# Optimization experiments

Measured on AMD Instinct MI355X. Metric: run time of the kernel, lower is better.

The kernel has to match this reference:

```python
import jax, jax.numpy as jnp
import numpy as np

BLOCK_SIZE = 128  # init_kwargs block_size


def setup_inputs() -> dict:
    key = jax.random.key(0)
    kq, kk, kv = jax.random.split(key, 3)
    shape = (8, 16, 4096, 128)  # [B, H, L, D]
    q = jax.random.normal(kq, shape, dtype=jnp.float32)
    k = jax.random.normal(kk, shape, dtype=jnp.float32)
    v = jax.random.normal(kv, shape, dtype=jnp.float32)
    return {"q": q, "k": k, "v": v}


def reference(q, k, v):
    # Block-diagonal local attention. The torch code builds a dense [L,L]
    # score matrix filled with -10000 off the block diagonal; exp(-10000)
    # underflows to exactly 0 in fp32 after max-subtraction, so the dense
    # softmax is mathematically identical to per-block softmax. We honor
    # the block sparsity and never materialize the L x L matrix.
    w = BLOCK_SIZE
    B, H, L, D = q.shape
    nb = L // w
    qb = q.reshape(B, H, nb, w, D)
    kb = k.reshape(B, H, nb, w, D)
    vb = v.reshape(B, H, nb, w, D)
    # NOTE: original applies NO 1/sqrt(D) scaling.
    score = jnp.einsum('bhnwd,bhnud->bhnwu', qb, kb)   # [B,H,nb,w,w]
    probs = jax.nn.softmax(score, axis=-1)
    out = jnp.einsum('bhnwu,bhnud->bhnwd', probs, vb)
    return out.reshape(B, H, L, D)
```

## Files before the change

kernel.cpp:

```cpp
#include <hip/hip_runtime.h>

typedef _Float16 half8  __attribute__((ext_vector_type(8)));
typedef _Float16 half4v __attribute__((ext_vector_type(4)));
typedef float    f32x4  __attribute__((ext_vector_type(4)));

__device__ __forceinline__ int swz(int row) {
    return ((row ^ (row >> 3)) & 15) << 4;
}

__global__ __launch_bounds__(512, 4) void battn_kernel(
    const float* __restrict__ Q, const float* __restrict__ K,
    const float* __restrict__ V, float* __restrict__ O)
{
    extern __shared__ __align__(16) char smem[];
    const int tid  = threadIdx.x;
    const int lane = tid & 63;
    const int w    = tid >> 6;
    const int la   = lane & 15;
    const int u    = lane >> 4;
    const size_t base = (size_t)blockIdx.x * (128 * 128);

    const float* Qb = Q + base;
    const float* Kb = K + base;
    const float* Vb = V + base;
    float*       Ob = O + base;

    float4 kreg[8];
#pragma unroll
    for (int it = 0; it < 8; ++it)
        kreg[it] = *(const float4*)(Kb + it * 2048 + tid * 4);

    half8 qfrag[4];
    {
        const float* qrow = Qb + (w * 16 + la) * 128;
#pragma unroll
        for (int kk = 0; kk < 4; ++kk) {
            const float4 a = *(const float4*)(qrow + kk * 32 + u * 8);
            const float4 b = *(const float4*)(qrow + kk * 32 + u * 8 + 4);
            qfrag[kk][0] = (_Float16)a.x; qfrag[kk][1] = (_Float16)a.y;
            qfrag[kk][2] = (_Float16)a.z; qfrag[kk][3] = (_Float16)a.w;
            qfrag[kk][4] = (_Float16)b.x; qfrag[kk][5] = (_Float16)b.y;
            qfrag[kk][6] = (_Float16)b.z; qfrag[kk][7] = (_Float16)b.w;
        }
    }
#pragma unroll
    for (int it = 0; it < 8; ++it) {
        const int idx = it * 2048 + tid * 4;
        const int row = idx >> 7;
        const int col = idx & 127;
        half4v h;
        h[0] = (_Float16)kreg[it].x; h[1] = (_Float16)kreg[it].y;
        h[2] = (_Float16)kreg[it].z; h[3] = (_Float16)kreg[it].w;
        int byte = row * 256 + col * 2;
        byte ^= swz(row);
        *(half4v*)(smem + byte) = h;
    }
    __syncthreads();

    float vld[32];
#pragma unroll
    for (int kk = 0; kk < 4; ++kk)
#pragma unroll
        for (int i = 0; i < 8; ++i)
            vld[kk * 8 + i] = Vb[(kk * 32 + u * 8 + i) * 128 + w * 16 + la];
    __builtin_amdgcn_sched_barrier(0);

    f32x4 acc[8];
#pragma unroll
    for (int t = 0; t < 8; ++t) acc[t] = (f32x4){0.f, 0.f, 0.f, 0.f};
#pragma unroll
    for (int t = 0; t < 8; ++t) {
#pragma unroll
        for (int kk = 0; kk < 4; ++kk) {
            const int row = t * 16 + la;
            int byte = row * 256 + kk * 64 + u * 16;
            byte ^= swz(row);
            const half8 kf = *(const half8*)(smem + byte);
            acc[t] = __builtin_amdgcn_mfma_f32_16x16x32_f16(qfrag[kk], kf, acc[t], 0, 0, 0);
        }
    }

    float inv[4];
#pragma unroll
    for (int r = 0; r < 4; ++r) {
        float m = acc[0][r];
#pragma unroll
        for (int t = 1; t < 8; ++t) m = fmaxf(m, acc[t][r]);
        m = fmaxf(m, __shfl_xor(m, 1));
        m = fmaxf(m, __shfl_xor(m, 2));
        m = fmaxf(m, __shfl_xor(m, 4));
        m = fmaxf(m, __shfl_xor(m, 8));
        float s = 0.f;
#pragma unroll
        for (int t = 0; t < 8; ++t) {
            const float e = __expf(acc[t][r] - m);
            acc[t][r] = e;
            s += e;
        }
        s += __shfl_xor(s, 1);
        s += __shfl_xor(s, 2);
        s += __shfl_xor(s, 4);
        s += __shfl_xor(s, 8);
        inv[r] = 1.0f / s;
    }

    half8 vfrag[4];
#pragma unroll
    for (int kk = 0; kk < 4; ++kk)
#pragma unroll
        for (int i = 0; i < 8; ++i)
            vfrag[kk][i] = (_Float16)vld[kk * 8 + i];

#pragma unroll
    for (int t = 0; t < 8; ++t) {
#pragma unroll
        for (int r = 0; r < 4; ++r) {
            const int q   = w * 16 + u * 4 + r;
            const int col = t * 16 + la;
            int byte = 32768 + q * 256 + col * 2;
            byte ^= swz(q & 15);
            *(_Float16*)(smem + byte) = (_Float16)(acc[t][r] * inv[r]);
        }
    }
    __syncthreads();

#pragma unroll
    for (int qt = 0; qt < 8; ++qt) {
        half8 pb[4];
#pragma unroll
        for (int kk = 0; kk < 4; ++kk) {
            int byte = 32768 + (qt * 16 + la) * 256 + kk * 64 + u * 16;
            byte ^= swz(la);
            pb[kk] = *(const half8*)(smem + byte);
        }
        f32x4 oa = (f32x4){0.f, 0.f, 0.f, 0.f};
#pragma unroll
        for (int kk = 0; kk < 4; ++kk)
            oa = __builtin_amdgcn_mfma_f32_16x16x32_f16(vfrag[kk], pb[kk], oa, 0, 0, 0);
        *(float4*)(Ob + (qt * 16 + la) * 128 + w * 16 + u * 4) =
            make_float4(oa[0], oa[1], oa[2], oa[3]);
    }
}

extern "C" void kernel_launch(void* const* d_in, const int* in_sizes, int n_in,
                              void* d_out, int out_size, void* d_ws, size_t ws_size,
                              hipStream_t stream) {
    const float* q = (const float*)d_in[0];
    const float* k = (const float*)d_in[1];
    const float* v = (const float*)d_in[2];
    float* o = (float*)d_out;
    const int nblocks = in_sizes[0] / (128 * 128);
    battn_kernel<<<dim3(nblocks), dim3(512), 65536, stream>>>(q, k, v, o);
}
```

Measured before the change: 214.7 us.

## Make workgroups loop over 16 blocks with register prefetch of next Q/K

Each workgroup now processes 16 consecutive 128x128 attention blocks in a loop instead of one. While the current block is computed, the next block's Q and K are loaded into registers with inline-asm global loads, gated by hand-placed s_waitcnt vmcnt counts. The goal is to hide global-load latency and amortize launch and setup cost. In exchange the grid shrinks to about one workgroup per CU, launch bounds drop to 2 blocks per CU, and shared memory becomes static. That leaves less wave-level parallelism to cover memory latency, and correctness depends on the manual vmcnt bookkeeping.

```diff
diff --git a/kernel.cpp b/kernel.cpp
--- a/kernel.cpp
+++ b/kernel.cpp
@@ -4,141 +4,192 @@
 typedef _Float16 half4v __attribute__((ext_vector_type(4)));
 typedef float    f32x4  __attribute__((ext_vector_type(4)));
 
+#define ITER 16
+
 __device__ __forceinline__ int swz(int row) {
     return ((row ^ (row >> 3)) & 15) << 4;
 }
 
-__global__ __launch_bounds__(512, 4) void battn_kernel(
+__device__ __forceinline__ half8 cvt_pair(f32x4 a, f32x4 b) {
+    half8 h;
+    h[0] = (_Float16)a[0]; h[1] = (_Float16)a[1]; h[2] = (_Float16)a[2]; h[3] = (_Float16)a[3];
+    h[4] = (_Float16)b[0]; h[5] = (_Float16)b[1]; h[6] = (_Float16)b[2]; h[7] = (_Float16)b[3];
+    return h;
+}
+
+__global__ __launch_bounds__(512, 2) void battn_kernel(
     const float* __restrict__ Q, const float* __restrict__ K,
     const float* __restrict__ V, float* __restrict__ O)
 {
-    extern __shared__ __align__(16) char smem[];
+    __shared__ __align__(16) char smem[65536];
     const int tid  = threadIdx.x;
     const int lane = tid & 63;
     const int w    = tid >> 6;
     const int la   = lane & 15;
     const int u    = lane >> 4;
-    const size_t base = (size_t)blockIdx.x * (128 * 128);
-
-    const float* Qb = Q + base;
-    const float* Kb = K + base;
-    const float* Vb = V + base;
-    float*       Ob = O + base;
-
-    float4 kreg[8];
-#pragma unroll
-    for (int it = 0; it < 8; ++it)
-        kreg[it] = *(const float4*)(Kb + it * 2048 + tid * 4);
-
+
+    const size_t base0 = (size_t)blockIdx.x * ITER * (128 * 128);
+
+    f32x4 kreg[8];
+    f32x4 qld[8];
+    float vld[32];
     half8 qfrag[4];
+
     {
-        const float* qrow = Qb + (w * 16 + la) * 128;
+        const float* qrow = Q + base0 + (w * 16 + la) * 128;
 #pragma unroll
         for (int kk = 0; kk < 4; ++kk) {
-            const float4 a = *(const float4*)(qrow + kk * 32 + u * 8);
-            const float4 b = *(const float4*)(qrow + kk * 32 + u * 8 + 4);
-            qfrag[kk][0] = (_Float16)a.x; qfrag[kk][1] = (_Float16)a.y;
-            qfrag[kk][2] = (_Float16)a.z; qfrag[kk][3] = (_Float16)a.w;
-            qfrag[kk][4] = (_Float16)b.x; qfrag[kk][5] = (_Float16)b.y;
-            qfrag[kk][6] = (_Float16)b.z; qfrag[kk][7] = (_Float16)b.w;
+            const float* p0 = qrow + kk * 32 + u * 8;
+            asm volatile("global_load_dwordx4 %0, %1, off" : "=v"(qld[2 * kk])     : "v"(p0));
+            asm volatile("global_load_dwordx4 %0, %1, off" : "=v"(qld[2 * kk + 1]) : "v"(p0 + 4));
+        }
+        const float* kptr = K + base0 + tid * 4;
+#pragma unroll
+        for (int it = 0; it < 8; ++it) {
+            const float* p = kptr + it * 2048;
+            asm volatile("global_load_dwordx4 %0, %1, off" : "=v"(kreg[it]) : "v"(p));
         }
     }
-#pragma unroll
-    for (int it = 0; it < 8; ++it) {
-        const int idx = it * 2048 + tid * 4;
-        const int row = idx >> 7;
-        const int col = idx & 127;
-        half4v h;
-        h[0] = (_Float16)kreg[it].x; h[1] = (_Float16)kreg[it].y;
-        h[2] = (_Float16)kreg[it].z; h[3] = (_Float16)kreg[it].w;
-        int byte = row * 256 + col * 2;
-        byte ^= swz(row);
-        *(half4v*)(smem + byte) = h;
-    }
-    __syncthreads();
-
-    float vld[32];
-#pragma unroll
-    for (int kk = 0; kk < 4; ++kk)
-#pragma unroll
-        for (int i = 0; i < 8; ++i)
-            vld[kk * 8 + i] = Vb[(kk * 32 + u * 8 + i) * 128 + w * 16 + la];
+    asm volatile("s_waitcnt vmcnt(8)" ::: "memory");
     __builtin_amdgcn_sched_barrier(0);
-
-    f32x4 acc[8];
-#pragma unroll
-    for (int t = 0; t < 8; ++t) acc[t] = (f32x4){0.f, 0.f, 0.f, 0.f};
-#pragma unroll
-    for (int t = 0; t < 8; ++t) {
-#pragma unroll
-        for (int kk = 0; kk < 4; ++kk) {
+#pragma unroll
+    for (int kk = 0; kk < 4; ++kk) qfrag[kk] = cvt_pair(qld[2 * kk], qld[2 * kk + 1]);
+    asm volatile("s_waitcnt vmcnt(0)" ::: "memory");
+    __builtin_amdgcn_sched_barrier(0);
+
+    for (int i = 0; i < ITER; ++i) {
+        const size_t base  = base0 + (size_t)i * (128 * 128);
+        const size_t nbase = base0 + (size_t)(i + 1 < ITER ? i + 1 : i) * (128 * 128);
+        float* Ob = O + base;
+
+#pragma unroll
+        for (int it = 0; it < 8; ++it) {
+            const int idx = it * 2048 + tid * 4;
+            const int row = idx >> 7;
+            const int col = idx & 127;
+            half4v h;
+            h[0] = (_Float16)kreg[it][0]; h[1] = (_Float16)kreg[it][1];
+            h[2] = (_Float16)kreg[it][2]; h[3] = (_Float16)kreg[it][3];
+            int byte = row * 256 + col * 2;
+            byte ^= swz(row);
+            *(half4v*)(smem + byte) = h;
+        }
+
+        {
+            const float* vbase = V + base + w * 16 + la;
+#pragma unroll
+            for (int kk = 0; kk < 4; ++kk)
+#pragma unroll
+                for (int t2 = 0; t2 < 8; ++t2) {
+                    const float* p = vbase + (kk * 32 + u * 8 + t2) * 128;
+                    asm volatile("global_load_dword %0, %1, off"
+                                 : "=v"(vld[kk * 8 + t2]) : "v"(p));
+                }
+        }
+        {
+            const float* qrow = Q + nbase + (w * 16 + la) * 128;
+#pragma unroll
+            for (int kk = 0; kk < 4; ++kk) {
+                const float* p0 = qrow + kk * 32 + u * 8;
+                asm volatile("global_load_dwordx4 %0, %1, off" : "=v"(qld[2 * kk])     : "v"(p0));
+                asm volatile("global_load_dwordx4 %0, %1, off" : "=v"(qld[2 * kk + 1]) : "v"(p0 + 4));
+            }
+            const float* kptr = K + nbase + tid * 4;
+#pragma unroll
+            for (int it = 0; it < 8; ++it) {
+                const float* p = kptr + it * 2048;
+                asm volatile("global_load_dwordx4 %0, %1, off" : "=v"(kreg[it]) : "v"(p));
+            }
+        }
+        __builtin_amdgcn_sched_barrier(0);
+
+        __syncthreads();
+
+        f32x4 acc[8];
+#pragma unroll
+        for (int t = 0; t < 8; ++t) acc[t] = (f32x4){0.f, 0.f, 0.f, 0.f};
+#pragma unroll
+        for (int t = 0; t < 8; ++t) {
             const int row = t * 16 + la;
-            int byte = row * 256 + kk * 64 + u * 16;
-            byte ^= swz(row);
-            const half8 kf = *(const half8*)(smem + byte);
-            acc[t] = __builtin_amdgcn_mfma_f32_16x16x32_f16(qfrag[kk], kf, acc[t], 0, 0, 0);
-        }
-    }
-
-    float inv[4];
-#pragma unroll
-    for (int r = 0; r < 4; ++r) {
-        float m = acc[0][r];
-#pragma unroll
-        for (int t = 1; t < 8; ++t) m = fmaxf(m, acc[t][r]);
-        m = fmaxf(m, __shfl_xor(m, 1));
-        m = fmaxf(m, __shfl_xor(m, 2));
-        m = fmaxf(m, __shfl_xor(m, 4));
-        m = fmaxf(m, __shfl_xor(m, 8));
-        float s = 0.f;
+#pragma unroll
+            for (int kk = 0; kk < 4; ++kk) {
+                int byte = row * 256 + kk * 64 + u * 16;
+                byte ^= swz(row);
+                const half8 kf = *(const half8*)(smem + byte);
+                acc[t] = __builtin_amdgcn_mfma_f32_16x16x32_f16(qfrag[kk], kf, acc[t], 0, 0, 0);
+            }
+        }
+
+        float inv[4];
+#pragma unroll
+        for (int r = 0; r < 4; ++r) {
+            float m = acc[0][r];
+#pragma unroll
+            for (int t = 1; t < 8; ++t) m = fmaxf(m, acc[t][r]);
+            m = fmaxf(m, __shfl_xor(m, 1));
+            m = fmaxf(m, __shfl_xor(m, 2));
+            m = fmaxf(m, __shfl_xor(m, 4));
+            m = fmaxf(m, __shfl_xor(m, 8));
+            float s = 0.f;
+#pragma unroll
+            for (int t = 0; t < 8; ++t) {
+                const float e = __expf(acc[t][r] - m);
+                acc[t][r] = e;
+                s += e;
+            }
+            s += __shfl_xor(s, 1);
+            s += __shfl_xor(s, 2);
+            s += __shfl_xor(s, 4);
+            s += __shfl_xor(s, 8);
+            inv[r] = 1.0f / s;
+        }
+
 #pragma unroll
         for (int t = 0; t < 8; ++t) {
-            const float e = __expf(acc[t][r] - m);
-            acc[t][r] = e;
-            s += e;
-        }
-        s += __shfl_xor(s, 1);
-        s += __shfl_xor(s, 2);
-        s += __shfl_xor(s, 4);
-        s += __shfl_xor(s, 8);
-        inv[r] = 1.0f / s;
-    }
-
-    half8 vfrag[4];
-#pragma unroll
-    for (int kk = 0; kk < 4; ++kk)
-#pragma unroll
-        for (int i = 0; i < 8; ++i)
-            vfrag[kk][i] = (_Float16)vld[kk * 8 + i];
-
-#pragma unroll
-    for (int t = 0; t < 8; ++t) {
-#pragma unroll
-        for (int r = 0; r < 4; ++r) {
-            const int q   = w * 16 + u * 4 + r;
-            const int col = t * 16 + la;
-            int byte = 32768 + q * 256 + col * 2;
-            byte ^= swz(q & 15);
-            *(_Float16*)(smem + byte) = (_Float16)(acc[t][r] * inv[r]);
-        }
-    }
-    __syncthreads();
-
-#pragma unroll
-    for (int qt = 0; qt < 8; ++qt) {
-        half8 pb[4];
-#pragma unroll
-        for (int kk = 0; kk < 4; ++kk) {
-            int byte = 32768 + (qt * 16 + la) * 256 + kk * 64 + u * 16;
-            byte ^= swz(la);
-            pb[kk] = *(const half8*)(smem + byte);
-        }
-        f32x4 oa = (f32x4){0.f, 0.f, 0.f, 0.f};
+#pragma unroll
+            for (int r = 0; r < 4; ++r) {
+                const int q   = w * 16 + u * 4 + r;
+                const int col = t * 16 + la;
+                int byte = 32768 + q * 256 + col * 2;
+                byte ^= swz(q & 15);
+                *(_Float16*)(smem + byte) = (_Float16)(acc[t][r] * inv[r]);
+            }
+        }
+        __syncthreads();
+
+        asm volatile("s_waitcnt vmcnt(16)" ::: "memory");
+        __builtin_amdgcn_sched_barrier(0);
+        half8 vfrag[4];
 #pragma unroll
         for (int kk = 0; kk < 4; ++kk)
-            oa = __builtin_amdgcn_mfma_f32_16x16x32_f16(vfrag[kk], pb[kk], oa, 0, 0, 0);
-        *(float4*)(Ob + (qt * 16 + la) * 128 + w * 16 + u * 4) =
-            make_float4(oa[0], oa[1], oa[2], oa[3]);
+#pragma unroll
+            for (int t2 = 0; t2 < 8; ++t2)
+                vfrag[kk][t2] = (_Float16)vld[kk * 8 + t2];
+
+#pragma unroll
+        for (int qt = 0; qt < 8; ++qt) {
+            half8 pb[4];
+#pragma unroll
+            for (int kk = 0; kk < 4; ++kk) {
+                int byte = 32768 + (qt * 16 + la) * 256 + kk * 64 + u * 16;
+                byte ^= swz(la);
+                pb[kk] = *(const half8*)(smem + byte);
+            }
+            f32x4 oa = (f32x4){0.f, 0.f, 0.f, 0.f};
+#pragma unroll
+            for (int kk = 0; kk < 4; ++kk)
+                oa = __builtin_amdgcn_mfma_f32_16x16x32_f16(vfrag[kk], pb[kk], oa, 0, 0, 0);
+            *(float4*)(Ob + (qt * 16 + la) * 128 + w * 16 + u * 4) =
+                make_float4(oa[0], oa[1], oa[2], oa[3]);
+        }
+
+        asm volatile("s_waitcnt vmcnt(16)" ::: "memory");
+        __builtin_amdgcn_sched_barrier(0);
+#pragma unroll
+        for (int kk = 0; kk < 4; ++kk) qfrag[kk] = cvt_pair(qld[2 * kk], qld[2 * kk + 1]);
+
+        asm volatile("s_waitcnt vmcnt(8)" ::: "memory");
+        __builtin_amdgcn_sched_barrier(0);
     }
 }
 
@@ -150,5 +201,6 @@
     const float* v = (const float*)d_in[2];
     float* o = (float*)d_out;
     const int nblocks = in_sizes[0] / (128 * 128);
-    battn_kernel<<<dim3(nblocks), dim3(512), 65536, stream>>>(q, k, v, o);
-}
+    const int nwg = nblocks / ITER;
+    battn_kernel<<<dim3(nwg), dim3(512), 0, stream>>>(q, k, v, o);
+}
```

New measurement: 221.3 us. +3.0%, slower.
